# Optimization experiments

Hardware: AMD Instinct MI355X
Metric: run time of the kernel (lower is better)

## Reference

```python
import jax, jax.numpy as jnp
import numpy as np
import math

OVERLAP_RATIO = 0.5
TAU_OVERLAP = 0.07
TAU_TILE = 0.2
TILE_LOSS_WEIGHT = 0.1


def setup_inputs() -> dict:
    key = jax.random.key(0)
    k1, k2 = jax.random.split(key)
    B, V, S, D = 8, 8, 576, 768
    z1 = jax.random.normal(k1, (B * V, S, D), dtype=jnp.float32)
    z2 = jax.random.normal(k2, (B * V, S, D), dtype=jnp.float32)
    # module expects L2-normalised projections
    z1 = z1 / jnp.linalg.norm(z1, axis=-1, keepdims=True)
    z2 = z2 / jnp.linalg.norm(z2, axis=-1, keepdims=True)
    return {"z1": z1, "z2": z2, "batch_size": B, "num_views": V}


def _sym_infonce_diag(logits):
    # logits: [..., N, N]; labels are the diagonal (same index positives).
    lse_q = jax.nn.logsumexp(logits, axis=-1)  # row-wise (q -> k)
    lse_k = jax.nn.logsumexp(logits, axis=-2)  # col-wise (k -> q), no transpose copy
    diag = jnp.diagonal(logits, axis1=-2, axis2=-1)
    return 0.5 * (jnp.mean(lse_q - diag) + jnp.mean(lse_k - diag))


def reference(z1, z2, batch_size, num_views):
    B, V = batch_size, num_views
    z1 = z1.astype(jnp.float32)
    z2 = z2.astype(jnp.float32)
    BV, S, D = z1.shape
    H = W = int(math.isqrt(S))

    # ---- overlap InfoNCE (circular adjacency) ----
    g1 = z1.reshape(B, V, H, W, D)
    g2 = z2.reshape(B, V, H, W, D)
    k = max(1, int(W * OVERLAP_RATIO))
    N = B * H * k
    curr_right = g1[:, :, :, -k:, :]                      # [B,V,H,k,D]
    next_left = jnp.roll(g2, -1, axis=1)[:, :, :, :k, :]  # [B,V,H,k,D]
    Q = jnp.transpose(curr_right, (1, 0, 2, 3, 4)).reshape(V, N, D)
    K = jnp.transpose(next_left, (1, 0, 2, 3, 4)).reshape(V, N, D)
    ov_logits = jnp.einsum('vnd,vmd->vnm', Q, K) / TAU_OVERLAP  # [V,N,N]
    L_overlap = _sym_infonce_diag(ov_logits)

    # ---- within-tile InfoNCE ----
    tile_logits = jnp.einsum('bsd,btd->bst', z1, z2) / TAU_TILE  # [BV,S,S]
    L_tile = _sym_infonce_diag(tile_logits)

    total = L_overlap + TILE_LOSS_WEIGHT * L_tile
    return total
```

## Files before the change

### kernel.cpp

```cpp
#include <hip/hip_runtime.h>
#include <hip/hip_bf16.h>

typedef __attribute__((ext_vector_type(8))) short bf16x8_t;
typedef __attribute__((ext_vector_type(4))) float f32x4_t;
typedef __attribute__((ext_vector_type(8))) unsigned short u16x8_t;

__device__ inline unsigned short bfr(float f) {
    __hip_bfloat16 h = __float2bfloat16(f);
    return *reinterpret_cast<unsigned short*>(&h);
}

__device__ inline u16x8_t cvt8(float4 x, float4 y) {
    u16x8_t v;
    v[0] = bfr(x.x); v[1] = bfr(x.y); v[2] = bfr(x.z); v[3] = bfr(x.w);
    v[4] = bfr(y.x); v[5] = bfr(y.y); v[6] = bfr(y.z); v[7] = bfr(y.w);
    return v;
}

__global__ __launch_bounds__(256, 2) void gemm128_lse_all(
    const float* __restrict__ z1, const float* __restrict__ z2,
    float* __restrict__ ws) {
    const int tid  = threadIdx.x;
    const int lane = tid & 63;
    const int w    = tid >> 6;
    const int wM   = w >> 1;
    const int wN   = w & 1;
    const int lr   = lane & 15;
    const int lg   = lane >> 4;

    const int bid = blockIdx.x;
    const int lb  = (bid & 7) * 524 + (bid >> 3);

    int M, TM, batch, rem;
    float inv_tau;
    float *rs, *cs, *dg;
    bool ov = (lb < 2592);
    if (ov) {
        M = 2304; TM = 18; inv_tau = 1.0f / 0.07f;
        rs = ws; cs = ws + 18432; dg = ws + 36864;
        batch = lb / 324; rem = lb - batch * 324;
    } else {
        M = 576; TM = 5; inv_tau = 1.0f / 0.2f;
        rs = ws + 55296; cs = ws + 92160; dg = ws + 129024;
        int tl = lb - 2592;
        batch = tl / 25; rem = tl - batch * 25;
    }
    const int brow = rem / TM;
    const int bcol = rem - brow * TM;

    __shared__ unsigned short smem[16384];
    __shared__ int offA[128], offB[128];

    if (tid < 128) {
        int r = brow * 128 + tid;
        int off;
        if (ov) {
            int b = r / 288, rm = r % 288, h = rm / 12, j = rm % 12;
            off = ((b * 8 + batch) * 576 + h * 24 + 12 + j) * 768;
        } else {
            off = ((r < M) ? (batch * 576 + r) : (batch * 576)) * 768;
        }
        offA[tid] = off;
    } else {
        int c = bcol * 128 + (tid - 128);
        int off;
        if (ov) {
            int b = c / 288, rm = c % 288, h = rm / 12, j = rm % 12;
            off = ((b * 8 + ((batch + 1) & 7)) * 576 + h * 24 + j) * 768;
        } else {
            off = ((c < M) ? (batch * 576 + c) : (batch * 576)) * 768;
        }
        offB[tid - 128] = off;
    }
    __syncthreads();

    const int lrow8 = lane >> 3;
    const int cswz  = (((lane & 7) ^ lrow8) << 3);
    int sA[4], sB[4], dA[4], dB[4];
#pragma unroll
    for (int ra = 0; ra < 4; ++ra) {
        sA[ra] = offA[w * 32 + ra * 8 + lrow8] + cswz;
        sB[ra] = offB[w * 32 + ra * 8 + lrow8] + cswz;
        dA[ra] = (w * 32 + ra * 8) * 64 + lane * 8;
        dB[ra] = 8192 + (w * 32 + ra * 8) * 64 + lane * 8;
    }

    int aoff[2][4], boff[2][4];
#pragma unroll
    for (int h = 0; h < 2; ++h) {
#pragma unroll
        for (int i = 0; i < 4; ++i) {
            int ra = wM * 64 + i * 16 + lr;
            aoff[h][i] = ra * 64 + (((h * 4 + lg) ^ (ra & 7)) << 3);
            int rb = wN * 64 + i * 16 + lr;
            boff[h][i] = 8192 + rb * 64 + (((h * 4 + lg) ^ (rb & 7)) << 3);
        }
    }

    f32x4_t acc[4][4];
#pragma unroll
    for (int i = 0; i < 4; ++i)
#pragma unroll
        for (int j = 0; j < 4; ++j) acc[i][j] = (f32x4_t){0.f, 0.f, 0.f, 0.f};

#define LOADT(T, fa, fb) do { \
    const int k0_ = (T) * 64; \
    _Pragma("unroll") \
    for (int ra = 0; ra < 4; ++ra) { \
        fa[2 * ra]     = *(const float4*)(z1 + sA[ra] + k0_); \
        fa[2 * ra + 1] = *(const float4*)(z1 + sA[ra] + k0_ + 4); \
        fb[2 * ra]     = *(const float4*)(z2 + sB[ra] + k0_); \
        fb[2 * ra + 1] = *(const float4*)(z2 + sB[ra] + k0_ + 4); \
    } } while (0)

#define WRT(fa, fb) do { \
    _Pragma("unroll") \
    for (int ra = 0; ra < 4; ++ra) { \
        *(u16x8_t*)&smem[dA[ra]] = cvt8(fa[2 * ra], fa[2 * ra + 1]); \
        *(u16x8_t*)&smem[dB[ra]] = cvt8(fb[2 * ra], fb[2 * ra + 1]); \
    } } while (0)

#define COMPUTE() do { \
    _Pragma("unroll") \
    for (int h = 0; h < 2; ++h) { \
        bf16x8_t av[4], bv[4]; \
        _Pragma("unroll") \
        for (int i = 0; i < 4; ++i) av[i] = *(const bf16x8_t*)&smem[aoff[h][i]]; \
        _Pragma("unroll") \
        for (int j = 0; j < 4; ++j) bv[j] = *(const bf16x8_t*)&smem[boff[h][j]]; \
        __builtin_amdgcn_s_setprio(1); \
        _Pragma("unroll") \
        for (int i = 0; i < 4; ++i) \
            _Pragma("unroll") \
            for (int j = 0; j < 4; ++j) \
                acc[i][j] = __builtin_amdgcn_mfma_f32_16x16x32_bf16( \
                    av[i], bv[j], acc[i][j], 0, 0, 0); \
        __builtin_amdgcn_s_setprio(0); \
    } } while (0)

    float4 a0[8], b0[8], a1[8], b1[8];
    LOADT(0, a0, b0);
#pragma unroll
    for (int tt = 0; tt < 6; ++tt) {
        const int t = 2 * tt;
        WRT(a0, b0);
        __syncthreads();
        LOADT(t + 1, a1, b1);
        COMPUTE();
        __syncthreads();
        WRT(a1, b1);
        __syncthreads();
        if (t + 2 < 12) LOADT(t + 2, a0, b0);
        COMPUTE();
        __syncthreads();
    }
#undef LOADT
#undef WRT
#undef COMPUTE

    const int rowbase = brow * 128 + wM * 64;
    const int colbase = bcol * 128 + wN * 64;
    float colacc[4] = {0.f, 0.f, 0.f, 0.f};
#pragma unroll
    for (int i = 0; i < 4; ++i) {
#pragma unroll
        for (int reg = 0; reg < 4; ++reg) {
            int row = rowbase + i * 16 + lg * 4 + reg;
            bool rv = row < M;
            float rp = 0.f;
#pragma unroll
            for (int j = 0; j < 4; ++j) {
                int col = colbase + j * 16 + lr;
                float L = acc[i][j][reg] * inv_tau;
                float e = (rv && (col < M)) ? __expf(L) : 0.f;
                rp += e;
                colacc[j] += e;
                if (rv && row == col) dg[batch * M + row] = L;
            }
#pragma unroll
            for (int s = 1; s < 16; s <<= 1) rp += __shfl_xor(rp, s);
            if (lr == 0 && rv) atomicAdd(&rs[batch * M + row], rp);
        }
    }
#pragma unroll
    for (int j = 0; j < 4; ++j) {
        float cv = colacc[j];
        cv += __shfl_xor(cv, 16);
        cv += __shfl_xor(cv, 32);
        int col = colbase + j * 16 + lr;
        if (lg == 0 && col < M) atomicAdd(&cs[batch * M + col], cv);
    }
}

__global__ __launch_bounds__(256) void finalize_kernel(
    const float* __restrict__ ws, float* __restrict__ out) {
    const float* rs_ov = ws;
    const float* cs_ov = ws + 18432;
    const float* dg_ov = ws + 36864;
    const float* rs_t  = ws + 55296;
    const float* cs_t  = ws + 92160;
    const float* dg_t  = ws + 129024;
    const int g0 = blockIdx.x * blockDim.x + threadIdx.x;
    const int gs = gridDim.x * blockDim.x;
    float s_ov = 0.f, s_t = 0.f;
    for (int i = g0; i < 18432; i += gs)
        s_ov += logf(rs_ov[i]) + logf(cs_ov[i]) - 2.f * dg_ov[i];
    for (int i = g0; i < 36864; i += gs)
        s_t += logf(rs_t[i]) + logf(cs_t[i]) - 2.f * dg_t[i];
    float c = 0.5f * s_ov / 18432.f + 0.05f * s_t / 36864.f;
#pragma unroll
    for (int s = 1; s < 64; s <<= 1) c += __shfl_xor(c, s);
    __shared__ float red[4];
    int wv = threadIdx.x >> 6;
    if ((threadIdx.x & 63) == 0) red[wv] = c;
    __syncthreads();
    if (threadIdx.x == 0)
        atomicAdd(out, red[0] + red[1] + red[2] + red[3]);
}

extern "C" void kernel_launch(void* const* d_in, const int* in_sizes, int n_in,
                              void* d_out, int out_size, void* d_ws, size_t ws_size,
                              hipStream_t stream) {
    const float* z1 = (const float*)d_in[0];
    const float* z2 = (const float*)d_in[1];
    float* out = (float*)d_out;
    float* ws  = (float*)d_ws;

    const size_t ACC_B = 165888 * sizeof(float);
    hipMemsetAsync(d_ws, 0, ACC_B, stream);
    hipMemsetAsync(d_out, 0, sizeof(float), stream);

    gemm128_lse_all<<<4192, 256, 0, stream>>>(z1, z2, ws);
    finalize_kernel<<<8, 256, 0, stream>>>(ws, out);
}
```

Baseline: 231.4 us.

## Drop register prefetch pipeline for higher occupancy and swizzle overlap tile order

Replaces the double-buffered register prefetch of global tiles with a simple load-convert-store-sync-compute loop, which frees many registers. The launch bound rises to 3 blocks per CU to use them. The overlap block mapping is regrouped into 6-column super-columns so that concurrently running blocks share B tiles in cache. Global load latency is no longer hidden inside a block and must instead be covered by the extra resident blocks.

Measured after the change: 194.8 us. 1.19x faster.

```diff
diff --git a/kernel.cpp b/kernel.cpp
--- a/kernel.cpp
+++ b/kernel.cpp
@@ -17,7 +17,7 @@
     return v;
 }
 
-__global__ __launch_bounds__(256, 2) void gemm128_lse_all(
+__global__ __launch_bounds__(256, 3) void gemm128_lse_all(
     const float* __restrict__ z1, const float* __restrict__ z2,
     float* __restrict__ ws) {
     const int tid  = threadIdx.x;
@@ -31,22 +31,27 @@
     const int bid = blockIdx.x;
     const int lb  = (bid & 7) * 524 + (bid >> 3);
 
-    int M, TM, batch, rem;
+    int M, batch, brow, bcol;
     float inv_tau;
     float *rs, *cs, *dg;
     bool ov = (lb < 2592);
     if (ov) {
-        M = 2304; TM = 18; inv_tau = 1.0f / 0.07f;
+        M = 2304; inv_tau = 1.0f / 0.07f;
         rs = ws; cs = ws + 18432; dg = ws + 36864;
-        batch = lb / 324; rem = lb - batch * 324;
+        batch = lb / 324;
+        int rem = lb - batch * 324;
+        int sc = rem / 108, r2 = rem - sc * 108;
+        brow = r2 / 6;
+        bcol = sc * 6 + (r2 - brow * 6);
     } else {
-        M = 576; TM = 5; inv_tau = 1.0f / 0.2f;
+        M = 576; inv_tau = 1.0f / 0.2f;
         rs = ws + 55296; cs = ws + 92160; dg = ws + 129024;
         int tl = lb - 2592;
-        batch = tl / 25; rem = tl - batch * 25;
-    }
-    const int brow = rem / TM;
-    const int bcol = rem - brow * TM;
+        batch = tl / 25;
+        int rem = tl - batch * 25;
+        brow = rem / 5;
+        bcol = rem - brow * 5;
+    }
 
     __shared__ unsigned short smem[16384];
     __shared__ int offA[128], offB[128];
@@ -103,60 +108,49 @@
 #pragma unroll
         for (int j = 0; j < 4; ++j) acc[i][j] = (f32x4_t){0.f, 0.f, 0.f, 0.f};
 
-#define LOADT(T, fa, fb) do { \
-    const int k0_ = (T) * 64; \
-    _Pragma("unroll") \
-    for (int ra = 0; ra < 4; ++ra) { \
-        fa[2 * ra]     = *(const float4*)(z1 + sA[ra] + k0_); \
-        fa[2 * ra + 1] = *(const float4*)(z1 + sA[ra] + k0_ + 4); \
-        fb[2 * ra]     = *(const float4*)(z2 + sB[ra] + k0_); \
-        fb[2 * ra + 1] = *(const float4*)(z2 + sB[ra] + k0_ + 4); \
-    } } while (0)
-
-#define WRT(fa, fb) do { \
-    _Pragma("unroll") \
-    for (int ra = 0; ra < 4; ++ra) { \
-        *(u16x8_t*)&smem[dA[ra]] = cvt8(fa[2 * ra], fa[2 * ra + 1]); \
-        *(u16x8_t*)&smem[dB[ra]] = cvt8(fb[2 * ra], fb[2 * ra + 1]); \
-    } } while (0)
-
-#define COMPUTE() do { \
-    _Pragma("unroll") \
-    for (int h = 0; h < 2; ++h) { \
-        bf16x8_t av[4], bv[4]; \
-        _Pragma("unroll") \
-        for (int i = 0; i < 4; ++i) av[i] = *(const bf16x8_t*)&smem[aoff[h][i]]; \
-        _Pragma("unroll") \
-        for (int j = 0; j < 4; ++j) bv[j] = *(const bf16x8_t*)&smem[boff[h][j]]; \
-        __builtin_amdgcn_s_setprio(1); \
-        _Pragma("unroll") \
-        for (int i = 0; i < 4; ++i) \
-            _Pragma("unroll") \
-            for (int j = 0; j < 4; ++j) \
-                acc[i][j] = __builtin_amdgcn_mfma_f32_16x16x32_bf16( \
-                    av[i], bv[j], acc[i][j], 0, 0, 0); \
-        __builtin_amdgcn_s_setprio(0); \
-    } } while (0)
-
-    float4 a0[8], b0[8], a1[8], b1[8];
-    LOADT(0, a0, b0);
-#pragma unroll
-    for (int tt = 0; tt < 6; ++tt) {
-        const int t = 2 * tt;
-        WRT(a0, b0);
+    for (int t = 0; t < 12; ++t) {
+        const int k0 = t * 64;
+        {
+            float4 fa[8];
+#pragma unroll
+            for (int ra = 0; ra < 4; ++ra) {
+                fa[2 * ra]     = *(const float4*)(z1 + sA[ra] + k0);
+                fa[2 * ra + 1] = *(const float4*)(z1 + sA[ra] + k0 + 4);
+            }
+#pragma unroll
+            for (int ra = 0; ra < 4; ++ra)
+                *(u16x8_t*)&smem[dA[ra]] = cvt8(fa[2 * ra], fa[2 * ra + 1]);
+        }
+        {
+            float4 fb[8];
+#pragma unroll
+            for (int ra = 0; ra < 4; ++ra) {
+                fb[2 * ra]     = *(const float4*)(z2 + sB[ra] + k0);
+                fb[2 * ra + 1] = *(const float4*)(z2 + sB[ra] + k0 + 4);
+            }
+#pragma unroll
+            for (int ra = 0; ra < 4; ++ra)
+                *(u16x8_t*)&smem[dB[ra]] = cvt8(fb[2 * ra], fb[2 * ra + 1]);
+        }
         __syncthreads();
-        LOADT(t + 1, a1, b1);
-        COMPUTE();
+#pragma unroll
+        for (int h = 0; h < 2; ++h) {
+            bf16x8_t av[4], bv[4];
+#pragma unroll
+            for (int i = 0; i < 4; ++i) av[i] = *(const bf16x8_t*)&smem[aoff[h][i]];
+#pragma unroll
+            for (int j = 0; j < 4; ++j) bv[j] = *(const bf16x8_t*)&smem[boff[h][j]];
+            __builtin_amdgcn_s_setprio(1);
+#pragma unroll
+            for (int i = 0; i < 4; ++i)
+#pragma unroll
+                for (int j = 0; j < 4; ++j)
+                    acc[i][j] = __builtin_amdgcn_mfma_f32_16x16x32_bf16(
+                        av[i], bv[j], acc[i][j], 0, 0, 0);
+            __builtin_amdgcn_s_setprio(0);
+        }
         __syncthreads();
-        WRT(a1, b1);
-        __syncthreads();
-        if (t + 2 < 12) LOADT(t + 2, a0, b0);
-        COMPUTE();
-        __syncthreads();
-    }
-#undef LOADT
-#undef WRT
-#undef COMPUTE
+    }
 
     const int rowbase = brow * 128 + wM * 64;
     const int colbase = bcol * 128 + wN * 64;
```
